# Performance work log

Hardware: AMD Instinct MI355X
Metric: run time of the kernel (lower is better)

Reference implementation:

```python
import jax, jax.numpy as jnp
import numpy as np

ALPHA = 0.01  # LeakyReLU negative slope

def _leaky(x):
    return jnp.where(x > 0, x, ALPHA * x)

def _conv(x, w, b):
    # x: NHWC, w: HWIO, valid padding, stride 1
    return jax.lax.conv_general_dilated(x, w, (1, 1), 'VALID',
        dimension_numbers=('NHWC', 'HWIO', 'NHWC')) + b

def _maxpool2(x):
    return jax.lax.reduce_window(x, -jnp.inf, jax.lax.max,
        (1, 2, 2, 1), (1, 2, 2, 1), 'VALID')

def setup_inputs() -> dict:
    key = jax.random.key(0)
    ks = jax.random.split(key, 32)
    B, S, H = 32, 197, 256
    FLAT = 47 * 62 * 64  # after conv/pool trunk = 186496
    def w(k, shape, fan_in):
        return jax.random.normal(k, shape, dtype=jnp.float32) * np.float32(1.0 / np.sqrt(fan_in))
    inp = {
        'x': jax.random.normal(ks[0], (B, S, H), dtype=jnp.float32),
        'conv1_w': w(ks[1], (3, 3, 1, 32), 9), 'conv1_b': jnp.zeros((32,), jnp.float32),
        'conv2_w': w(ks[2], (3, 3, 32, 64), 288), 'conv2_b': jnp.zeros((64,), jnp.float32),
        'w_c1': w(ks[3], (FLAT, 512), FLAT), 'b_c1': jnp.zeros((512,), jnp.float32),
        'w_c2': w(ks[4], (512, 256), 512), 'b_c2': jnp.zeros((256,), jnp.float32),
        'w_co': w(ks[5], (256, 225 * 13), 256), 'b_co': jnp.zeros((225 * 13,), jnp.float32),
        'w_sm': w(ks[6], (13, 13), 13), 'b_sm': jnp.zeros((13,), jnp.float32),
        'w_r1': w(ks[7], (FLAT, 256), FLAT), 'b_r1': jnp.zeros((256,), jnp.float32),
        'w_r2': w(ks[8], (256, 128), 256), 'b_r2': jnp.zeros((128,), jnp.float32),
        'w_r3': w(ks[9], (128, 128), 128), 'b_r3': jnp.zeros((128,), jnp.float32),
        'w_r4': w(ks[10], (128, 64), 128), 'b_r4': jnp.zeros((64,), jnp.float32),
        'w_ro': w(ks[11], (64, 225 * 4), 64), 'b_ro': jnp.zeros((225 * 4,), jnp.float32),
        'w_sg': w(ks[12], (4, 4), 4), 'b_sg': jnp.zeros((4,), jnp.float32),
    }
    return inp

def reference(x, conv1_w, conv1_b, conv2_w, conv2_b,
              w_c1, b_c1, w_c2, b_c2, w_co, b_co, w_sm, b_sm,
              w_r1, b_r1, w_r2, b_r2, w_r3, b_r3, w_r4, b_r4,
              w_ro, b_ro, w_sg, b_sg):
    # CNN trunk on expanded hidden state (B, S, H, 1)
    h = x[..., None]
    h = jax.nn.relu(_conv(h, conv1_w, conv1_b))
    h = _maxpool2(h)
    h = jax.nn.relu(_conv(h, conv2_w, conv2_b))
    h = _maxpool2(h)
    h = h.reshape(h.shape[0], -1)  # (B, 186496)
    # classification branch (dropout is identity at inference)
    y = _leaky(h @ w_c1 + b_c1)
    y = _leaky(y @ w_c2 + b_c2)
    y = _leaky(y @ w_co + b_co).reshape(-1, 225, 13)
    # 225-step loop of shared Dense(13, softmax) heads -> one batched matmul
    class_out = jax.nn.softmax(jnp.einsum('bpi,ij->bpj', y, w_sm) + b_sm, axis=-1)
    z = _leaky(h @ w_r1 + b_r1)
    z = _leaky(z @ w_r2 + b_r2)
    z = _leaky(z @ w_r3 + b_r3)
    z = _leaky(z @ w_r4 + b_r4)
    z = (z @ w_ro + b_ro).reshape(-1, 225, 4)
    reg_out = jax.nn.sigmoid(jnp.einsum('bpi,ij->bpj', z, w_sg) + b_sg)
    return class_out, reg_out
```

## Files before the change

### kernel.cpp

```cpp
#include <hip/hip_runtime.h>
#include <hip/hip_bf16.h>

#define ALPHA 0.01f

typedef __attribute__((ext_vector_type(8))) __bf16 bf16x8;
typedef __attribute__((ext_vector_type(4))) float f32x4;

#define BATCH 32
#define P1H 97
#define P1W 127
#define P2W 62
#define FLAT 186496
#define GK 512
#define NGK 365
#define PSTRIDE1 16448
#define PSTRIDE2 8256
#define CONV1_BLOCKS 1540

static __device__ __forceinline__ unsigned short f2bf(float x) {
  union { float f; unsigned u; } c; c.f = x;
  unsigned r = c.u + 0x7fffu + ((c.u >> 16) & 1u);
  return (unsigned short)(r >> 16);
}

static __device__ __forceinline__ unsigned pack2bf(float lo, float hi) {
  union { float f; unsigned u; } a, b;
  a.f = lo; b.f = hi;
  unsigned ra = (a.u + 0x7fffu + ((a.u >> 16) & 1u)) >> 16;
  unsigned rb = (b.u + 0x7fffu + ((b.u >> 16) & 1u)) & 0xffff0000u;
  return ra | rb;
}

__global__ __launch_bounds__(256) void conv1_pool(const float* __restrict__ x,
    const float* __restrict__ w1, const float* __restrict__ b1,
    unsigned short* __restrict__ p1,
    const float* __restrict__ w2, unsigned short* __restrict__ bpack) {
  if (blockIdx.x >= CONV1_BLOCKS) {
    int o = (blockIdx.x - CONV1_BLOCKS) * 256 + threadIdx.x;
    if (o < 9 * 4 * 512) {
      int f = o >> 9;
      int within = o & 511;
      int lane = within >> 3, j = within & 7;
      int tap = f >> 2, nf = f & 3;
      int k = ((lane >> 4) << 3) + j;
      int n = nf * 16 + (lane & 15);
      bpack[o] = f2bf(w2[(tap * 32 + k) * 64 + n]);
    }
    return;
  }
  int pid = blockIdx.x * 256 + threadIdx.x;
  if (pid >= BATCH * P1H * P1W) return;
  int b = pid / (P1H * P1W);
  int rem = pid - b * (P1H * P1W);
  int ph = rem / P1W;
  int pw = rem - ph * P1W;
  const float* xb = x + ((b * 197 + 2 * ph) * 256 + 2 * pw);
  float in[4][4];
#pragma unroll
  for (int r = 0; r < 4; ++r) {
    float2 v0 = *reinterpret_cast<const float2*>(xb + r * 256);
    float2 v1 = *reinterpret_cast<const float2*>(xb + r * 256 + 2);
    in[r][0] = v0.x; in[r][1] = v0.y; in[r][2] = v1.x; in[r][3] = v1.y;
  }
  unsigned pk[16];
#pragma unroll
  for (int c = 0; c < 32; ++c) {
    float s00 = b1[c], s01 = s00, s10 = s00, s11 = s00;
#pragma unroll
    for (int ky = 0; ky < 3; ++ky)
#pragma unroll
      for (int kx = 0; kx < 3; ++kx) {
        float w = w1[(ky * 3 + kx) * 32 + c];
        s00 = fmaf(in[ky][kx], w, s00);
        s01 = fmaf(in[ky][kx + 1], w, s01);
        s10 = fmaf(in[ky + 1][kx], w, s10);
        s11 = fmaf(in[ky + 1][kx + 1], w, s11);
      }
    float m = fmaxf(fmaxf(s00, s01), fmaxf(s10, s11));
    m = fmaxf(m, 0.0f);
    unsigned short u = f2bf(m);
    if (c & 1) pk[c >> 1] |= ((unsigned)u) << 16;
    else pk[c >> 1] = (unsigned)u;
  }
  uint4* dst = reinterpret_cast<uint4*>(p1 + (size_t)pid * 32);
#pragma unroll
  for (int g = 0; g < 4; ++g)
    dst[g] = make_uint4(pk[g * 4], pk[g * 4 + 1], pk[g * 4 + 2], pk[g * 4 + 3]);
}

__global__ __launch_bounds__(256) void conv2_pool(const unsigned short* __restrict__ p1,
    const unsigned short* __restrict__ bpack, const float* __restrict__ b2,
    unsigned short* __restrict__ hbf) {
  __shared__ alignas(16) unsigned char lds_buf[65536];
  int prow = blockIdx.x, b = blockIdx.y;
  int tid = threadIdx.x;
  int lane = tid & 63, wid = tid >> 6;
  {
    const uint4* src = reinterpret_cast<const uint4*>(bpack);
    uint4* dst = reinterpret_cast<uint4*>(lds_buf);
    for (int i = tid; i < 2304; i += 256) dst[i] = src[i];
  }
  __syncthreads();
  int row = lane & 15, kg = lane >> 4;
  int rowbase[4];
  int coff[4][3];
#pragma unroll
  for (int mf = 0; mf < 4; ++mf) {
    int m = wid * 64 + mf * 16 + row;
    int cro = m >> 7, cc = m & 127;
    rowbase[mf] = ((b * 97 + 2 * prow + cro) * 127) * 32 + kg * 8;
#pragma unroll
    for (int kx = 0; kx < 3; ++kx) {
      int ic = cc + kx; if (ic > 126) ic = 126;
      coff[mf][kx] = ic * 32;
    }
  }
  f32x4 acc[4][4];
#pragma unroll
  for (int i = 0; i < 4; ++i)
#pragma unroll
    for (int j = 0; j < 4; ++j) acc[i][j] = (f32x4){0.f, 0.f, 0.f, 0.f};

  const bf16x8* bl = reinterpret_cast<const bf16x8*>(lds_buf);
#pragma unroll
  for (int ky = 0; ky < 3; ++ky) {
#pragma unroll
    for (int kx = 0; kx < 3; ++kx) {
      int tap = ky * 3 + kx;
      bf16x8 a[4];
#pragma unroll
      for (int mf = 0; mf < 4; ++mf) {
        int addr = rowbase[mf] + ky * (127 * 32) + coff[mf][kx];
        a[mf] = *reinterpret_cast<const bf16x8*>(p1 + addr);
      }
      bf16x8 bf[4];
#pragma unroll
      for (int nf = 0; nf < 4; ++nf) bf[nf] = bl[(tap * 4 + nf) * 64 + lane];
#pragma unroll
      for (int nf = 0; nf < 4; ++nf)
#pragma unroll
        for (int mf = 0; mf < 4; ++mf)
          acc[mf][nf] = __builtin_amdgcn_mfma_f32_16x16x32_bf16(a[mf], bf[nf], acc[mf][nf], 0, 0, 0);
    }
  }
  __syncthreads();
  float* stage = reinterpret_cast<float*>(lds_buf);
#pragma unroll
  for (int mf = 0; mf < 4; ++mf)
#pragma unroll
    for (int nf = 0; nf < 4; ++nf) {
      int ch = nf * 16 + (lane & 15);
      float bias = b2[ch];
#pragma unroll
      for (int j = 0; j < 4; ++j) {
        int m = wid * 64 + mf * 16 + (lane >> 4) * 4 + j;
        float v = acc[mf][nf][j] + bias;
        stage[m * 64 + ch] = fmaxf(v, 0.f);
      }
    }
  __syncthreads();
  unsigned short* hb = hbf + (size_t)b * FLAT + prow * (P2W * 64);
  for (int o = tid; o < P2W * 64; o += 256) {
    int pw = o >> 6, ch = o & 63;
    int c0 = 2 * pw;
    float v = fmaxf(fmaxf(stage[c0 * 64 + ch], stage[(c0 + 1) * 64 + ch]),
                    fmaxf(stage[(128 + c0) * 64 + ch], stage[(129 + c0) * 64 + ch]));
    hb[o] = f2bf(v);
  }
}

template <int N, int CSTRIDE>
__global__ __launch_bounds__(256, 6) void gemm_mfma(const float* __restrict__ W,
    const unsigned short* __restrict__ hbf, float* __restrict__ part) {
  int kc = blockIdx.y;
  int n0 = blockIdx.x * 128;
  int t = threadIdx.x, lane = t & 63, wid = t >> 6;
  int k0 = kc * GK;
  int klen = FLAT - k0; if (klen > GK) klen = GK;
  int nsteps = klen >> 5;
  int cl = lane & 15, kg = lane >> 4;
  const float* Wb0 = W + (size_t)(k0 + kg * 8) * N + (n0 + wid * 32 + cl);
  const float* Wb1 = Wb0 + 16;
  const unsigned short* ha0 = hbf + (size_t)cl * FLAT + k0 + kg * 8;
  const unsigned short* ha1 = ha0 + (size_t)16 * FLAT;

  f32x4 acc[2][2];
#pragma unroll
  for (int i = 0; i < 2; ++i)
#pragma unroll
    for (int j = 0; j < 2; ++j) acc[i][j] = (f32x4){0.f, 0.f, 0.f, 0.f};

  float e0[8], e1[8];
  union U4 { unsigned u[4]; bf16x8 v; };
  U4 b0, b1;
  bf16x8 a0, a1, a0n, a1n;

  a0 = *reinterpret_cast<const bf16x8*>(ha0);
  a1 = *reinterpret_cast<const bf16x8*>(ha1);
#pragma unroll
  for (int j = 0; j < 8; ++j) {
    e0[j] = Wb0[(size_t)j * N];
    e1[j] = Wb1[(size_t)j * N];
  }
#pragma unroll
  for (int p = 0; p < 4; ++p) {
    b0.u[p] = pack2bf(e0[2 * p], e0[2 * p + 1]);
    b1.u[p] = pack2bf(e1[2 * p], e1[2 * p + 1]);
  }

  for (int kt = 0; kt < nsteps; ++kt) {
    bool pf = (kt + 1 < nsteps);
    if (pf) {
      a0n = *reinterpret_cast<const bf16x8*>(ha0 + (kt + 1) * 32);
      a1n = *reinterpret_cast<const bf16x8*>(ha1 + (kt + 1) * 32);
      const float* wp0 = Wb0 + (size_t)(kt + 1) * 32 * N;
      const float* wp1 = Wb1 + (size_t)(kt + 1) * 32 * N;
#pragma unroll
      for (int j = 0; j < 8; ++j) {
        e0[j] = wp0[(size_t)j * N];
        e1[j] = wp1[(size_t)j * N];
      }
    }
    acc[0][0] = __builtin_amdgcn_mfma_f32_16x16x32_bf16(a0, b0.v, acc[0][0], 0, 0, 0);
    acc[1][0] = __builtin_amdgcn_mfma_f32_16x16x32_bf16(a1, b0.v, acc[1][0], 0, 0, 0);
    acc[0][1] = __builtin_amdgcn_mfma_f32_16x16x32_bf16(a0, b1.v, acc[0][1], 0, 0, 0);
    acc[1][1] = __builtin_amdgcn_mfma_f32_16x16x32_bf16(a1, b1.v, acc[1][1], 0, 0, 0);
    if (pf) {
#pragma unroll
      for (int p = 0; p < 4; ++p) {
        b0.u[p] = pack2bf(e0[2 * p], e0[2 * p + 1]);
        b1.u[p] = pack2bf(e1[2 * p], e1[2 * p + 1]);
      }
      a0 = a0n; a1 = a1n;
    }
  }

  float* out = part + (size_t)kc * CSTRIDE;
#pragma unroll
  for (int mf = 0; mf < 2; ++mf)
#pragma unroll
    for (int nf = 0; nf < 2; ++nf)
#pragma unroll
      for (int j = 0; j < 4; ++j) {
        int m = mf * 16 + kg * 4 + j;
        int n = n0 + wid * 32 + nf * 16 + cl;
        out[m * N + n] = acc[mf][nf][j];
      }
}

__global__ __launch_bounds__(256) void reduce_big(const float* __restrict__ part1,
    const float* __restrict__ part2, const float* __restrict__ b_c1,
    const float* __restrict__ b_r1, float* __restrict__ y1, float* __restrict__ z1) {
  __shared__ float red[8][32];
  int b = blockIdx.x, t = threadIdx.x;
  int oo = t & 31, j = t >> 5;
  float s = 0.f;
  if (b < 512) {
    const float* p = part1 + b * 32 + oo;
    for (int c = j; c < NGK; c += 8) s += p[(size_t)c * PSTRIDE1];
    red[j][oo] = s;
    __syncthreads();
    if (t < 32) {
      float r = 0.f;
#pragma unroll
      for (int jj = 0; jj < 8; ++jj) r += red[jj][t];
      int o = b * 32 + t;
      r += b_c1[o & 511];
      y1[o] = r > 0.f ? r : ALPHA * r;
    }
  } else {
    const float* p = part2 + (b - 512) * 32 + oo;
    for (int c = j; c < NGK; c += 8) s += p[(size_t)c * PSTRIDE2];
    red[j][oo] = s;
    __syncthreads();
    if (t < 32) {
      float r = 0.f;
#pragma unroll
      for (int jj = 0; jj < 8; ++jj) r += red[jj][t];
      int u = (b - 512) * 32 + t;
      r += b_r1[u & 255];
      z1[u] = r > 0.f ? r : ALPHA * r;
    }
  }
}

__global__ __launch_bounds__(256) void tail_all(
    const float* __restrict__ y1g, const float* __restrict__ z1g,
    const float* __restrict__ w_c2, const float* __restrict__ b_c2,
    const float* __restrict__ w_co, const float* __restrict__ b_co,
    const float* __restrict__ w_sm, const float* __restrict__ b_sm,
    const float* __restrict__ w_r2, const float* __restrict__ b_r2,
    const float* __restrict__ w_r3, const float* __restrict__ b_r3,
    const float* __restrict__ w_r4, const float* __restrict__ b_r4,
    const float* __restrict__ w_ro, const float* __restrict__ b_ro,
    const float* __restrict__ w_sg, const float* __restrict__ b_sg,
    float* __restrict__ class_out, float* __restrict__ reg_out) {
  int tile = blockIdx.x, m = blockIdx.y, t = threadIdx.x;
  if (tile < 8) {
    __shared__ float ly1[512], ly2[256], ly3[29 * 13];
    ly1[t] = y1g[m * 512 + t];
    ly1[t + 256] = y1g[m * 512 + 256 + t];
    __syncthreads();
    {
      float s = b_c2[t];
      for (int k = 0; k < 512; ++k) s = fmaf(ly1[k], w_c2[k * 256 + t], s);
      ly2[t] = s > 0.f ? s : ALPHA * s;
    }
    __syncthreads();
    int p0 = tile * 29;
    int np = 225 - p0; if (np > 29) np = 29;
    int ncols = np * 13;
    for (int n = t; n < ncols; n += 256) {
      int col = p0 * 13 + n;
      float s = b_co[col];
      for (int k = 0; k < 256; ++k) s = fmaf(ly2[k], w_co[k * 2925 + col], s);
      ly3[n] = s > 0.f ? s : ALPHA * s;
    }
    __syncthreads();
    if (t < np) {
      float v[13], l[13], mx = -1e30f;
#pragma unroll
      for (int i = 0; i < 13; ++i) v[i] = ly3[t * 13 + i];
#pragma unroll
      for (int j = 0; j < 13; ++j) {
        float s = b_sm[j];
#pragma unroll
        for (int i = 0; i < 13; ++i) s = fmaf(v[i], w_sm[i * 13 + j], s);
        l[j] = s; mx = fmaxf(mx, s);
      }
      float sum = 0.f;
#pragma unroll
      for (int j = 0; j < 13; ++j) { l[j] = expf(l[j] - mx); sum += l[j]; }
      float inv = 1.f / sum;
      float* o = class_out + ((size_t)m * 225 + p0 + t) * 13;
#pragma unroll
      for (int j = 0; j < 13; ++j) o[j] = l[j] * inv;
    }
  } else {
    __shared__ float lz1[256], lz2[128], lz3[128], lz4[64], lzo[57 * 4];
    lz1[t] = z1g[m * 256 + t];
    __syncthreads();
    if (t < 128) {
      float s = b_r2[t];
      for (int k = 0; k < 256; ++k) s = fmaf(lz1[k], w_r2[k * 128 + t], s);
      lz2[t] = s > 0.f ? s : ALPHA * s;
    }
    __syncthreads();
    if (t < 128) {
      float s = b_r3[t];
      for (int k = 0; k < 128; ++k) s = fmaf(lz2[k], w_r3[k * 128 + t], s);
      lz3[t] = s > 0.f ? s : ALPHA * s;
    }
    __syncthreads();
    if (t < 64) {
      float s = b_r4[t];
      for (int k = 0; k < 128; ++k) s = fmaf(lz3[k], w_r4[k * 64 + t], s);
      lz4[t] = s > 0.f ? s : ALPHA * s;
    }
    __syncthreads();
    int p0 = (tile - 8) * 57;
    int np = 225 - p0; if (np > 57) np = 57;
    int ncols = np * 4;
    for (int n = t; n < ncols; n += 256) {
      int col = p0 * 4 + n;
      float s = b_ro[col];
#pragma unroll
      for (int k = 0; k < 64; ++k) s = fmaf(lz4[k], w_ro[k * 900 + col], s);
      lzo[n] = s;
    }
    __syncthreads();
    if (t < np) {
      float z[4];
#pragma unroll
      for (int i = 0; i < 4; ++i) z[i] = lzo[t * 4 + i];
      float* ro = reg_out + ((size_t)m * 225 + p0 + t) * 4;
#pragma unroll
      for (int j = 0; j < 4; ++j) {
        float s = b_sg[j];
#pragma unroll
        for (int i = 0; i < 4; ++i) s = fmaf(z[i], w_sg[i * 4 + j], s);
        ro[j] = 1.f / (1.f + expf(-s));
      }
    }
  }
}

#define OFF_P1     ((size_t)0)
#define OFF_BPACK  ((size_t)25229312)
#define OFF_H      ((size_t)25266176)
#define OFF_PART1  ((size_t)37201920)
#define OFF_PART2  ((size_t)61216000)
#define OFF_Y1     ((size_t)73269760)
#define OFF_Z1     ((size_t)73335296)

extern "C" void kernel_launch(void* const* d_in, const int* in_sizes, int n_in,
                              void* d_out, int out_size, void* d_ws, size_t ws_size,
                              hipStream_t stream) {
  const float* x     = (const float*)d_in[0];
  const float* w1    = (const float*)d_in[1];
  const float* b1    = (const float*)d_in[2];
  const float* w2    = (const float*)d_in[3];
  const float* b2    = (const float*)d_in[4];
  const float* w_c1  = (const float*)d_in[5];
  const float* b_c1  = (const float*)d_in[6];
  const float* w_c2  = (const float*)d_in[7];
  const float* b_c2  = (const float*)d_in[8];
  const float* w_co  = (const float*)d_in[9];
  const float* b_co  = (const float*)d_in[10];
  const float* w_sm  = (const float*)d_in[11];
  const float* b_sm  = (const float*)d_in[12];
  const float* w_r1  = (const float*)d_in[13];
  const float* b_r1  = (const float*)d_in[14];
  const float* w_r2  = (const float*)d_in[15];
  const float* b_r2  = (const float*)d_in[16];
  const float* w_r3  = (const float*)d_in[17];
  const float* b_r3  = (const float*)d_in[18];
  const float* w_r4  = (const float*)d_in[19];
  const float* b_r4  = (const float*)d_in[20];
  const float* w_ro  = (const float*)d_in[21];
  const float* b_ro  = (const float*)d_in[22];
  const float* w_sg  = (const float*)d_in[23];
  const float* b_sg  = (const float*)d_in[24];

  char* ws = (char*)d_ws;
  unsigned short* p1    = (unsigned short*)(ws + OFF_P1);
  unsigned short* bpack = (unsigned short*)(ws + OFF_BPACK);
  unsigned short* hbf   = (unsigned short*)(ws + OFF_H);
  float*          part1 = (float*)(ws + OFF_PART1);
  float*          part2 = (float*)(ws + OFF_PART2);
  float*          y1    = (float*)(ws + OFF_Y1);
  float*          z1    = (float*)(ws + OFF_Z1);

  float* class_out = (float*)d_out;
  float* reg_out   = (float*)d_out + 32 * 225 * 13;

  conv1_pool<<<CONV1_BLOCKS + 72, 256, 0, stream>>>(x, w1, b1, p1, w2, bpack);
  conv2_pool<<<dim3(47, 32), 256, 0, stream>>>(p1, bpack, b2, hbf);
  gemm_mfma<512, PSTRIDE1><<<dim3(4, NGK), 256, 0, stream>>>(w_c1, hbf, part1);
  gemm_mfma<256, PSTRIDE2><<<dim3(2, NGK), 256, 0, stream>>>(w_r1, hbf, part2);
  reduce_big<<<768, 256, 0, stream>>>(part1, part2, b_c1, b_r1, y1, z1);
  tail_all<<<dim3(12, 32), 256, 0, stream>>>(y1, z1,
      w_c2, b_c2, w_co, b_co, w_sm, b_sm,
      w_r2, b_r2, w_r3, b_r3, w_r4, b_r4,
      w_ro, b_ro, w_sg, b_sg, class_out, reg_out);
}
```

Measured before the change: 270.9 us.

## Stage weight tiles through per-wave LDS with vectorized float4 loads in GEMM

```diff
diff --git a/kernel.cpp b/kernel.cpp
--- a/kernel.cpp
+++ b/kernel.cpp
@@ -170,8 +170,9 @@
 }
 
 template <int N, int CSTRIDE>
-__global__ __launch_bounds__(256, 6) void gemm_mfma(const float* __restrict__ W,
+__global__ __launch_bounds__(256, 5) void gemm_mfma(const float* __restrict__ W,
     const unsigned short* __restrict__ hbf, float* __restrict__ part) {
+  __shared__ alignas(16) unsigned lds[4 * 2 * 576];
   int kc = blockIdx.y;
   int n0 = blockIdx.x * 128;
   int t = threadIdx.x, lane = t & 63, wid = t >> 6;
@@ -179,8 +180,15 @@
   int klen = FLAT - k0; if (klen > GK) klen = GK;
   int nsteps = klen >> 5;
   int cl = lane & 15, kg = lane >> 4;
-  const float* Wb0 = W + (size_t)(k0 + kg * 8) * N + (n0 + wid * 32 + cl);
-  const float* Wb1 = Wb0 + 16;
+  int r8 = lane >> 3, q = lane & 7;
+  int nw = n0 + wid * 32;
+
+  const float* wsrc = W + (size_t)(k0 + r8) * N + nw + q * 4;
+  unsigned* lw = lds + wid * 1152;
+  unsigned* wbase = lw + r8 * 18 + 2 * q;
+  const unsigned* rbase = lw + kg * 144 + (cl >> 1);
+  int sh = (cl & 1) * 16;
+
   const unsigned short* ha0 = hbf + (size_t)cl * FLAT + k0 + kg * 8;
   const unsigned short* ha1 = ha0 + (size_t)16 * FLAT;
 
@@ -190,48 +198,58 @@
 #pragma unroll
     for (int j = 0; j < 2; ++j) acc[i][j] = (f32x4){0.f, 0.f, 0.f, 0.f};
 
-  float e0[8], e1[8];
   union U4 { unsigned u[4]; bf16x8 v; };
-  U4 b0, b1;
+  float4 st[4];
   bf16x8 a0, a1, a0n, a1n;
 
+#pragma unroll
+  for (int i = 0; i < 4; ++i)
+    st[i] = *reinterpret_cast<const float4*>(wsrc + (size_t)i * 8 * N);
   a0 = *reinterpret_cast<const bf16x8*>(ha0);
   a1 = *reinterpret_cast<const bf16x8*>(ha1);
 #pragma unroll
-  for (int j = 0; j < 8; ++j) {
-    e0[j] = Wb0[(size_t)j * N];
-    e1[j] = Wb1[(size_t)j * N];
-  }
-#pragma unroll
-  for (int p = 0; p < 4; ++p) {
-    b0.u[p] = pack2bf(e0[2 * p], e0[2 * p + 1]);
-    b1.u[p] = pack2bf(e1[2 * p], e1[2 * p + 1]);
-  }
-
+  for (int i = 0; i < 4; ++i) {
+    unsigned u0 = pack2bf(st[i].x, st[i].y);
+    unsigned u1 = pack2bf(st[i].z, st[i].w);
+    *reinterpret_cast<uint2*>(wbase + i * 144) = make_uint2(u0, u1);
+  }
+
+  int cur = 0;
   for (int kt = 0; kt < nsteps; ++kt) {
     bool pf = (kt + 1 < nsteps);
     if (pf) {
+      const float* ws = wsrc + (size_t)(kt + 1) * 32 * N;
+#pragma unroll
+      for (int i = 0; i < 4; ++i)
+        st[i] = *reinterpret_cast<const float4*>(ws + (size_t)i * 8 * N);
       a0n = *reinterpret_cast<const bf16x8*>(ha0 + (kt + 1) * 32);
       a1n = *reinterpret_cast<const bf16x8*>(ha1 + (kt + 1) * 32);
-      const float* wp0 = Wb0 + (size_t)(kt + 1) * 32 * N;
-      const float* wp1 = Wb1 + (size_t)(kt + 1) * 32 * N;
-#pragma unroll
-      for (int j = 0; j < 8; ++j) {
-        e0[j] = wp0[(size_t)j * N];
-        e1[j] = wp1[(size_t)j * N];
-      }
+    }
+    const unsigned* rb = rbase + cur * 576;
+    U4 b0, b1;
+#pragma unroll
+    for (int p = 0; p < 4; ++p) {
+      unsigned A0 = rb[p * 36];
+      unsigned B0 = rb[p * 36 + 18];
+      unsigned A1 = rb[p * 36 + 8];
+      unsigned B1 = rb[p * 36 + 18 + 8];
+      b0.u[p] = ((A0 >> sh) & 0xffffu) | (((B0 >> sh) & 0xffffu) << 16);
+      b1.u[p] = ((A1 >> sh) & 0xffffu) | (((B1 >> sh) & 0xffffu) << 16);
     }
     acc[0][0] = __builtin_amdgcn_mfma_f32_16x16x32_bf16(a0, b0.v, acc[0][0], 0, 0, 0);
     acc[1][0] = __builtin_amdgcn_mfma_f32_16x16x32_bf16(a1, b0.v, acc[1][0], 0, 0, 0);
     acc[0][1] = __builtin_amdgcn_mfma_f32_16x16x32_bf16(a0, b1.v, acc[0][1], 0, 0, 0);
     acc[1][1] = __builtin_amdgcn_mfma_f32_16x16x32_bf16(a1, b1.v, acc[1][1], 0, 0, 0);
     if (pf) {
-#pragma unroll
-      for (int p = 0; p < 4; ++p) {
-        b0.u[p] = pack2bf(e0[2 * p], e0[2 * p + 1]);
-        b1.u[p] = pack2bf(e1[2 * p], e1[2 * p + 1]);
+      unsigned* wb = wbase + (cur ^ 1) * 576;
+#pragma unroll
+      for (int i = 0; i < 4; ++i) {
+        unsigned u0 = pack2bf(st[i].x, st[i].y);
+        unsigned u1 = pack2bf(st[i].z, st[i].w);
+        *reinterpret_cast<uint2*>(wb + i * 144) = make_uint2(u0, u1);
       }
       a0 = a0n; a1 = a1n;
+      cur ^= 1;
     }
   }
 
```

Result: slower. 276.7 us (+2.1%).

## Stage weight tiles through LDS with float4 loads and widen GEMM N-tile

Applied to the files above, without the earlier changes.

```diff
diff --git a/kernel.cpp b/kernel.cpp
--- a/kernel.cpp
+++ b/kernel.cpp
@@ -16,6 +16,7 @@
 #define PSTRIDE1 16448
 #define PSTRIDE2 8256
 #define CONV1_BLOCKS 1540
+#define LPITCH 264
 
 static __device__ __forceinline__ unsigned short f2bf(float x) {
   union { float f; unsigned u; } c; c.f = x;
@@ -170,82 +171,68 @@
 }
 
 template <int N, int CSTRIDE>
-__global__ __launch_bounds__(256, 6) void gemm_mfma(const float* __restrict__ W,
+__global__ __launch_bounds__(256) void gemm_mfma(const float* __restrict__ W,
     const unsigned short* __restrict__ hbf, float* __restrict__ part) {
+  __shared__ alignas(16) unsigned lds[16 * LPITCH];
   int kc = blockIdx.y;
-  int n0 = blockIdx.x * 128;
-  int t = threadIdx.x, lane = t & 63, wid = t >> 6;
+  int n0 = blockIdx.x * 256;
+  int t = threadIdx.x, lane = t & 63, w = t >> 6;
   int k0 = kc * GK;
   int klen = FLAT - k0; if (klen > GK) klen = GK;
   int nsteps = klen >> 5;
   int cl = lane & 15, kg = lane >> 4;
-  const float* Wb0 = W + (size_t)(k0 + kg * 8) * N + (n0 + wid * 32 + cl);
-  const float* Wb1 = Wb0 + 16;
-  const unsigned short* ha0 = hbf + (size_t)cl * FLAT + k0 + kg * 8;
-  const unsigned short* ha1 = ha0 + (size_t)16 * FLAT;
-
-  f32x4 acc[2][2];
-#pragma unroll
-  for (int i = 0; i < 2; ++i)
-#pragma unroll
-    for (int j = 0; j < 2; ++j) acc[i][j] = (f32x4){0.f, 0.f, 0.f, 0.f};
-
-  float e0[8], e1[8];
-  union U4 { unsigned u[4]; bf16x8 v; };
-  U4 b0, b1;
-  bf16x8 a0, a1, a0n, a1n;
-
-  a0 = *reinterpret_cast<const bf16x8*>(ha0);
-  a1 = *reinterpret_cast<const bf16x8*>(ha1);
-#pragma unroll
-  for (int j = 0; j < 8; ++j) {
-    e0[j] = Wb0[(size_t)j * N];
-    e1[j] = Wb1[(size_t)j * N];
-  }
-#pragma unroll
-  for (int p = 0; p < 4; ++p) {
-    b0.u[p] = pack2bf(e0[2 * p], e0[2 * p + 1]);
-    b1.u[p] = pack2bf(e1[2 * p], e1[2 * p + 1]);
-  }
+  int mh = w & 1, nh = w >> 1;
+
+  const float* wsrc = W + (size_t)(k0 + w * 8) * N + n0 + lane * 4;
+  unsigned* lwb = lds + (w * 4) * LPITCH + lane * 4;
+  const unsigned short* ha = hbf + (size_t)(mh * 16 + cl) * FLAT + k0 + kg * 8;
+
+  f32x4 acc[8];
+#pragma unroll
+  for (int f = 0; f < 8; ++f) acc[f] = (f32x4){0.f, 0.f, 0.f, 0.f};
+
+  float4 st[8];
+#pragma unroll
+  for (int i = 0; i < 8; ++i)
+    st[i] = *reinterpret_cast<const float4*>(wsrc + (size_t)i * N);
 
   for (int kt = 0; kt < nsteps; ++kt) {
-    bool pf = (kt + 1 < nsteps);
-    if (pf) {
-      a0n = *reinterpret_cast<const bf16x8*>(ha0 + (kt + 1) * 32);
-      a1n = *reinterpret_cast<const bf16x8*>(ha1 + (kt + 1) * 32);
-      const float* wp0 = Wb0 + (size_t)(kt + 1) * 32 * N;
-      const float* wp1 = Wb1 + (size_t)(kt + 1) * 32 * N;
-#pragma unroll
-      for (int j = 0; j < 8; ++j) {
-        e0[j] = wp0[(size_t)j * N];
-        e1[j] = wp1[(size_t)j * N];
-      }
-    }
-    acc[0][0] = __builtin_amdgcn_mfma_f32_16x16x32_bf16(a0, b0.v, acc[0][0], 0, 0, 0);
-    acc[1][0] = __builtin_amdgcn_mfma_f32_16x16x32_bf16(a1, b0.v, acc[1][0], 0, 0, 0);
-    acc[0][1] = __builtin_amdgcn_mfma_f32_16x16x32_bf16(a0, b1.v, acc[0][1], 0, 0, 0);
-    acc[1][1] = __builtin_amdgcn_mfma_f32_16x16x32_bf16(a1, b1.v, acc[1][1], 0, 0, 0);
-    if (pf) {
-#pragma unroll
-      for (int p = 0; p < 4; ++p) {
-        b0.u[p] = pack2bf(e0[2 * p], e0[2 * p + 1]);
-        b1.u[p] = pack2bf(e1[2 * p], e1[2 * p + 1]);
-      }
-      a0 = a0n; a1 = a1n;
-    }
-  }
-
-  float* out = part + (size_t)kc * CSTRIDE;
-#pragma unroll
-  for (int mf = 0; mf < 2; ++mf)
-#pragma unroll
-    for (int nf = 0; nf < 2; ++nf)
-#pragma unroll
-      for (int j = 0; j < 4; ++j) {
-        int m = mf * 16 + kg * 4 + j;
-        int n = n0 + wid * 32 + nf * 16 + cl;
-        out[m * N + n] = acc[mf][nf][j];
-      }
+    __syncthreads();
+#pragma unroll
+    for (int ip = 0; ip < 4; ++ip) {
+      float4 lo = st[2 * ip], hi = st[2 * ip + 1];
+      *reinterpret_cast<uint4*>(lwb + ip * LPITCH) =
+          make_uint4(pack2bf(lo.x, hi.x), pack2bf(lo.y, hi.y),
+                     pack2bf(lo.z, hi.z), pack2bf(lo.w, hi.w));
+    }
+    __syncthreads();
+    if (kt + 1 < nsteps) {
+      const float* ws = wsrc + (size_t)(kt + 1) * 32 * N;
+#pragma unroll
+      for (int i = 0; i < 8; ++i)
+        st[i] = *reinterpret_cast<const float4*>(ws + (size_t)i * N);
+    }
+    bf16x8 a = *reinterpret_cast<const bf16x8*>(ha + kt * 32);
+#pragma unroll
+    for (int f = 0; f < 8; ++f) {
+      int col = nh * 128 + f * 16 + cl;
+      union { unsigned u[4]; bf16x8 v; } bb;
+#pragma unroll
+      for (int p = 0; p < 4; ++p)
+        bb.u[p] = lds[(kg * 4 + p) * LPITCH + col];
+      acc[f] = __builtin_amdgcn_mfma_f32_16x16x32_bf16(a, bb.v, acc[f], 0, 0, 0);
+    }
+  }
+
+  float* out = part + (size_t)kc * CSTRIDE + n0;
+#pragma unroll
+  for (int f = 0; f < 8; ++f)
+#pragma unroll
+    for (int j = 0; j < 4; ++j) {
+      int m = mh * 16 + kg * 4 + j;
+      int col = nh * 128 + f * 16 + cl;
+      out[m * N + col] = acc[f][j];
+    }
 }
 
 __global__ __launch_bounds__(256) void reduce_big(const float* __restrict__ part1,
@@ -436,8 +423,8 @@
 
   conv1_pool<<<CONV1_BLOCKS + 72, 256, 0, stream>>>(x, w1, b1, p1, w2, bpack);
   conv2_pool<<<dim3(47, 32), 256, 0, stream>>>(p1, bpack, b2, hbf);
-  gemm_mfma<512, PSTRIDE1><<<dim3(4, NGK), 256, 0, stream>>>(w_c1, hbf, part1);
-  gemm_mfma<256, PSTRIDE2><<<dim3(2, NGK), 256, 0, stream>>>(w_r1, hbf, part2);
+  gemm_mfma<512, PSTRIDE1><<<dim3(2, NGK), 256, 0, stream>>>(w_c1, hbf, part1);
+  gemm_mfma<256, PSTRIDE2><<<dim3(1, NGK), 256, 0, stream>>>(w_r1, hbf, part2);
   reduce_big<<<768, 256, 0, stream>>>(part1, part2, b_c1, b_r1, y1, z1);
   tail_all<<<dim3(12, 32), 256, 0, stream>>>(y1, z1,
       w_c2, b_c2, w_co, b_co, w_sm, b_sm,
```

Measured after the change: 257.1 us. 5.1% less time.
